# Kernel optimization log

Hardware: AMD Instinct MI355X
Metric: run time of the kernel (lower is better)

Reference implementation:

```python
import jax, jax.numpy as jnp
import numpy as np

EMBED_DIM = 768
NUM_HEADS = 12
HEAD_DIM = EMBED_DIM // NUM_HEADS


def setup_inputs() -> dict:
    key = jax.random.key(0)
    k1, k2, k3, k4, k5 = jax.random.split(key, 5)
    B, S, D = 2, 4096, EMBED_DIM
    scale = 1.0 / np.sqrt(D)
    return {
        "x": jax.random.normal(k1, (B, S, D), dtype=jnp.float32),
        "Wqkv": jax.random.normal(k2, (D, 3 * D), dtype=jnp.float32) * scale,
        "bqkv": jax.random.normal(k3, (3 * D,), dtype=jnp.float32) * 0.02,
        "Wout": jax.random.normal(k4, (D, D), dtype=jnp.float32) * scale,
        "bout": jax.random.normal(k5, (D,), dtype=jnp.float32) * 0.02,
    }


def reference(x, Wqkv, bqkv, Wout, bout):
    B, S, D = x.shape
    H, Hd = NUM_HEADS, HEAD_DIM
    # fused QKV projection: [B,S,3D]
    qkv = x @ Wqkv + bqkv
    q, k, v = jnp.split(qkv, 3, axis=-1)
    # [B,S,D] -> [B,H,S,Hd]
    q = q.reshape(B, S, H, Hd).transpose(0, 2, 1, 3)
    k = k.reshape(B, S, H, Hd).transpose(0, 2, 1, 3)
    v = v.reshape(B, S, H, Hd).transpose(0, 2, 1, 3)
    # causal SDPA (dropout_p = 0)
    scores = jnp.einsum("bhsd,bhtd->bhst", q, k) / jnp.sqrt(jnp.asarray(Hd, x.dtype))
    causal = jnp.tril(jnp.ones((S, S), dtype=bool))  # [S,S]
    scores = jnp.where(causal[None, None], scores, jnp.finfo(x.dtype).min)
    attn = jax.nn.softmax(scores, axis=-1)
    y = jnp.einsum("bhst,bhtd->bhsd", attn, v)  # [B,H,S,Hd]
    y = y.transpose(0, 2, 1, 3).reshape(B, S, D)
    return y @ Wout + bout
```

## Files before the change

kernel.cpp:

```cpp
#include <hip/hip_runtime.h>

#define S_LEN 4096
#define NH 12
#define HD 64
#define DMODEL 768
#define BATCH 2
#define MTOT (BATCH * S_LEN)

typedef __bf16 bf16x8 __attribute__((ext_vector_type(8)));
typedef __bf16 bf16x4 __attribute__((ext_vector_type(4)));
typedef float f32x4 __attribute__((ext_vector_type(4)));
typedef float f32x8 __attribute__((ext_vector_type(8)));

#define SM_SCALE_LOG2E 0.18033688f
#define SLAB_STRIDE 16896

__device__ __forceinline__ f32x4 f32x4_zero() {
  f32x4 z = {0.f, 0.f, 0.f, 0.f};
  return z;
}

__device__ __forceinline__ void async16(const __bf16* g, void* l) {
  __builtin_amdgcn_global_load_lds(
      (const __attribute__((address_space(1))) void*)g,
      (__attribute__((address_space(3))) void*)l, 16, 0, 0);
}

__global__ __launch_bounds__(256) void prep_all(const float* __restrict__ x,
                                                const float* __restrict__ Wqkv,
                                                const float* __restrict__ Wout,
                                                __bf16* __restrict__ xb,
                                                __bf16* __restrict__ Wqkv_t,
                                                __bf16* __restrict__ Wout_t) {
  __shared__ __bf16 t[64][72];
  const int bid = blockIdx.x;
  if (bid < 3072) {
    int i = bid * 256 + threadIdx.x;
    f32x8 a = ((const f32x8*)x)[i];
    bf16x8 o;
#pragma unroll
    for (int j = 0; j < 8; ++j) o[j] = (__bf16)a[j];
    ((bf16x8*)xb)[i] = o;
    return;
  }
  const float* in;
  __bf16* out;
  int N, v;
  if (bid < 3504) {
    in = Wqkv;
    out = Wqkv_t;
    N = 3 * DMODEL;
    v = bid - 3072;
  } else {
    in = Wout;
    out = Wout_t;
    N = DMODEL;
    v = bid - 3504;
  }
  int kb = (v % 12) * 64, nb = (v / 12) * 64;
  int c = threadIdx.x & 63, r0 = threadIdx.x >> 6;
#pragma unroll
  for (int i = 0; i < 16; ++i) {
    int r = r0 * 16 + i;
    t[c][r] = (__bf16)in[(size_t)(kb + r) * N + nb + c];
  }
  __syncthreads();
#pragma unroll
  for (int i = 0; i < 16; ++i) {
    int r = r0 * 16 + i;
    out[(size_t)(nb + r) * DMODEL + kb + c] = t[r][c];
  }
}

__device__ __forceinline__ void gemm128_bt(const __bf16* __restrict__ A,
                                           const __bf16* __restrict__ Bt,
                                           int m0, int n0, int K,
                                           __bf16* Alds, __bf16* Blds,
                                           f32x4 acc[4][4]) {
  const int tid = threadIdx.x;
  const int l = tid & 63, w = tid >> 6;
  const int wr = w >> 1, wc = w & 1;
  const int g = l >> 4, ln = l & 15;

  const int rr = tid >> 3;
  const int sx = (tid & 7) ^ (rr & 7);
  const __bf16* As = A + (size_t)(m0 + rr) * K + sx * 8;
  const __bf16* Bs = Bt + (size_t)(n0 + rr) * K + sx * 8;
  char* Ad = (char*)Alds + (w << 10);
  char* Bd = (char*)Blds + (w << 10);

  for (int k0 = 0; k0 < K; k0 += 64) {
#pragma unroll
    for (int i = 0; i < 4; ++i) {
      async16(As + (size_t)(i * 32) * K + k0, Ad + i * 4096);
      async16(Bs + (size_t)(i * 32) * K + k0, Bd + i * 4096);
    }
    __syncthreads();
#pragma unroll
    for (int kk = 0; kk < 2; ++kk) {
      bf16x8 af[4], bfr[4];
#pragma unroll
      for (int mi = 0; mi < 4; ++mi) {
        int row = wr * 64 + mi * 16 + ln;
        af[mi] = *(const bf16x8*)(Alds + row * 64 + ((((kk << 2) + g) ^ (row & 7)) << 3));
      }
#pragma unroll
      for (int ni = 0; ni < 4; ++ni) {
        int row = wc * 64 + ni * 16 + ln;
        bfr[ni] = *(const bf16x8*)(Blds + row * 64 + ((((kk << 2) + g) ^ (row & 7)) << 3));
      }
#pragma unroll
      for (int mi = 0; mi < 4; ++mi)
#pragma unroll
        for (int ni = 0; ni < 4; ++ni)
          acc[mi][ni] =
              __builtin_amdgcn_mfma_f32_16x16x32_bf16(af[mi], bfr[ni], acc[mi][ni], 0, 0, 0);
    }
    __syncthreads();
  }
}

__global__ __launch_bounds__(256) void gemm_qkv(const __bf16* __restrict__ xb,
                                                const __bf16* __restrict__ Wt,
                                                const float* __restrict__ bqkv,
                                                __bf16* __restrict__ Qo,
                                                __bf16* __restrict__ Ko,
                                                __bf16* __restrict__ Vto) {
  __shared__ __bf16 Alds[128 * 64];
  __shared__ __bf16 Blds[128 * 64];
  int bm = blockIdx.x & 63, bn = blockIdx.x >> 6;
  int m0 = bm * 128, n0 = bn * 128;
  f32x4 acc[4][4];
#pragma unroll
  for (int i = 0; i < 4; ++i)
#pragma unroll
    for (int j = 0; j < 4; ++j) acc[i][j] = f32x4_zero();
  gemm128_bt(xb, Wt, m0, n0, DMODEL, Alds, Blds, acc);

  const int l = threadIdx.x & 63, w = threadIdx.x >> 6;
  const int wr = w >> 1, wc = w & 1, g = l >> 4, ln = l & 15;
#pragma unroll
  for (int ni = 0; ni < 4; ++ni) {
    int ncol = n0 + wc * 64 + ni * 16 + ln;
    int which = ncol / DMODEL;
    int dd = ncol - which * DMODEL;
    int h = dd >> 6, hd = dd & 63;
    float bias = bqkv[ncol];
    if (which == 2) {
#pragma unroll
      for (int mi = 0; mi < 4; ++mi)
#pragma unroll
        for (int r = 0; r < 4; ++r) {
          int mrow = m0 + wr * 64 + mi * 16 + 4 * g + r;
          int b = mrow >> 12, s = mrow & (S_LEN - 1);
          float v = acc[mi][ni][r] + bias;
          Vto[(((size_t)(b * NH + h) * HD) + hd) * S_LEN + s] = (__bf16)v;
        }
    } else {
      __bf16* op = (which == 0) ? Qo : Ko;
      const float scl = (which == 0) ? SM_SCALE_LOG2E : 1.0f;
#pragma unroll
      for (int mi = 0; mi < 4; ++mi)
#pragma unroll
        for (int r = 0; r < 4; ++r) {
          int mrow = m0 + wr * 64 + mi * 16 + 4 * g + r;
          int b = mrow >> 12, s = mrow & (S_LEN - 1);
          float v = (acc[mi][ni][r] + bias) * scl;
          op[((((size_t)b * NH + h) * S_LEN) + s) * HD + hd] = (__bf16)v;
        }
    }
  }
}

__global__ __launch_bounds__(256) void gemm_out(const __bf16* __restrict__ yb,
                                                const __bf16* __restrict__ Wt,
                                                const float* __restrict__ bout,
                                                float* __restrict__ out) {
  __shared__ __bf16 Alds[128 * 64];
  __shared__ __bf16 Blds[128 * 64];
  int bm = blockIdx.x & 63, bn = blockIdx.x >> 6;
  int m0 = bm * 128, n0 = bn * 128;
  f32x4 acc[4][4];
#pragma unroll
  for (int i = 0; i < 4; ++i)
#pragma unroll
    for (int j = 0; j < 4; ++j) acc[i][j] = f32x4_zero();
  gemm128_bt(yb, Wt, m0, n0, DMODEL, Alds, Blds, acc);

  const int l = threadIdx.x & 63, w = threadIdx.x >> 6;
  const int wr = w >> 1, wc = w & 1, g = l >> 4, ln = l & 15;
#pragma unroll
  for (int ni = 0; ni < 4; ++ni) {
    int ncol = n0 + wc * 64 + ni * 16 + ln;
    float bias = bout[ncol];
#pragma unroll
    for (int mi = 0; mi < 4; ++mi)
#pragma unroll
      for (int r = 0; r < 4; ++r) {
        int mrow = m0 + wr * 64 + mi * 16 + 4 * g + r;
        out[(size_t)mrow * DMODEL + ncol] = acc[mi][ni][r] + bias;
      }
  }
}

__global__ __launch_bounds__(512) void attn_fwd18(const __bf16* __restrict__ Q,
                                                  const __bf16* __restrict__ K,
                                                  const __bf16* __restrict__ Vt,
                                                  __bf16* __restrict__ Y,
                                                  char* __restrict__ Po) {
  __shared__ __bf16 KVl[2][2][4096];
  __shared__ char Plb[8][2048];

  const int tid = threadIdx.x;
  const int wv = tid >> 6, l = tid & 63;
  const int g = l >> 4, ln = l & 15;
  const int bi = blockIdx.x;
  const int xcd = bi & 7, j = bi >> 3;
  const int head = xcd * 3 + (j % 3);
  const int r_ = j / 3;

  int c, part, np;
  bool split;
  if (r_ < 32) {
    c = 31 - (r_ >> 2);
    part = r_ & 3;
    np = 4;
    split = true;
  } else if (r_ < 56) {
    int q = r_ - 32;
    c = 23 - q / 3;
    part = q % 3;
    np = 3;
    split = true;
  } else if (r_ < 72) {
    int q = r_ - 56;
    c = 15 - (q >> 1);
    part = q & 1;
    np = 2;
    split = true;
  } else {
    c = 79 - r_;
    part = 0;
    np = 1;
    split = false;
  }
  const int T = 2 * c + 2;
  const int base = T / np, rem = T % np;
  const int t0 = part * base + (part < rem ? part : rem);
  const int t1 = t0 + base + (part < rem ? 1 : 0);

  const int q0 = 128 * c + 16 * wv;

  const size_t hb = (size_t)head * (S_LEN * HD);
  const __bf16* Qh = Q + hb;
  const __bf16* Kh = K + hb;
  const __bf16* Vh = Vt + hb;

  const int sw = (ln & 7) << 4;
  char* Pw = Plb[wv] + ln * 128;

  const int r0 = tid >> 3;
  const int s0 = (tid & 7) ^ (r0 & 7);
  const size_t kL = (size_t)r0 * HD + s0 * 8;
  const size_t vL = (size_t)r0 * S_LEN + s0 * 8;
  const int ldsoff = wv << 10;

  bf16x8 qf[2];
#pragma unroll
  for (int t = 0; t < 2; ++t)
    qf[t] = *(const bf16x8*)(Qh + (size_t)(q0 + ln) * HD + 32 * t + 8 * g);

  bf16x8 ones;
#pragma unroll
  for (int t = 0; t < 8; ++t) ones[t] = (__bf16)1.0f;

  f32x4 o[4], o5;
#pragma unroll
  for (int nt = 0; nt < 4; ++nt) o[nt] = f32x4_zero();
  o5 = f32x4_zero();

  const __bf16* kq = Kh + (size_t)t0 * 64 * HD;
  const __bf16* vq = Vh + t0 * 64;
  {
    async16(kq + kL, (char*)&KVl[0][0][0] + ldsoff);
    async16(vq + vL, (char*)&KVl[0][1][0] + ldsoff);
    __syncthreads();
  }
  kq += (size_t)64 * HD;
  vq += 64;

  int cur = 0;
  for (int i = t0; i < t1; ++i) {
    const bool more = (i + 1) < t1;
    if (more) {
      async16(kq + kL, (char*)&KVl[cur ^ 1][0][0] + ldsoff);
      async16(vq + vL, (char*)&KVl[cur ^ 1][1][0] + ldsoff);
      kq += (size_t)64 * HD;
      vq += 64;
    }

    const __bf16* Kl = &KVl[cur][0][0];
    const __bf16* Vl = &KVl[cur][1][0];
    const int rel = q0 - 64 * i;

    if (rel > -16) {
      if (rel >= 63) {
#pragma unroll
        for (int jt = 0; jt < 4; ++jt) {
          int row = 16 * jt + ln;
          bf16x8 kf0 = *(const bf16x8*)(Kl + row * 64 + ((g ^ (row & 7)) << 3));
          bf16x8 kf1 = *(const bf16x8*)(Kl + row * 64 + (((4 + g) ^ (row & 7)) << 3));
          f32x4 z = f32x4_zero();
          z = __builtin_amdgcn_mfma_f32_16x16x32_bf16(kf0, qf[0], z, 0, 0, 0);
          z = __builtin_amdgcn_mfma_f32_16x16x32_bf16(kf1, qf[1], z, 0, 0, 0);
          bf16x4 qd;
#pragma unroll
          for (int r = 0; r < 4; ++r) qd[r] = (__bf16)__builtin_exp2f(z[r]);
          *(bf16x4*)(Pw + ((32 * jt + 8 * g) ^ sw)) = qd;
        }
      } else {
        const int thr = rel + ln;
#pragma unroll
        for (int jt = 0; jt < 4; ++jt) {
          int row = 16 * jt + ln;
          bf16x8 kf0 = *(const bf16x8*)(Kl + row * 64 + ((g ^ (row & 7)) << 3));
          bf16x8 kf1 = *(const bf16x8*)(Kl + row * 64 + (((4 + g) ^ (row & 7)) << 3));
          f32x4 z = f32x4_zero();
          z = __builtin_amdgcn_mfma_f32_16x16x32_bf16(kf0, qf[0], z, 0, 0, 0);
          z = __builtin_amdgcn_mfma_f32_16x16x32_bf16(kf1, qf[1], z, 0, 0, 0);
          bf16x4 qd;
#pragma unroll
          for (int r = 0; r < 4; ++r) {
            float pv = __builtin_exp2f(z[r]);
            if (16 * jt + 4 * g + r > thr) pv = 0.f;
            qd[r] = (__bf16)pv;
          }
          *(bf16x4*)(Pw + ((32 * jt + 8 * g) ^ sw)) = qd;
        }
      }

      bf16x8 pa0 = *(const bf16x8*)(Pw + ((16 * g) ^ sw));
      bf16x8 pa1 = *(const bf16x8*)(Pw + ((64 + 16 * g) ^ sw));
      __builtin_amdgcn_s_setprio(1);
      o5 = __builtin_amdgcn_mfma_f32_16x16x32_bf16(pa0, ones, o5, 0, 0, 0);
      o5 = __builtin_amdgcn_mfma_f32_16x16x32_bf16(pa1, ones, o5, 0, 0, 0);
#pragma unroll
      for (int nt = 0; nt < 4; ++nt) {
        int row = 16 * nt + ln;
        bf16x8 vf0 = *(const bf16x8*)(Vl + row * 64 + ((g ^ (row & 7)) << 3));
        bf16x8 vf1 = *(const bf16x8*)(Vl + row * 64 + (((4 + g) ^ (row & 7)) << 3));
        o[nt] = __builtin_amdgcn_mfma_f32_16x16x32_bf16(pa0, vf0, o[nt], 0, 0, 0);
        o[nt] = __builtin_amdgcn_mfma_f32_16x16x32_bf16(pa1, vf1, o[nt], 0, 0, 0);
      }
      __builtin_amdgcn_s_setprio(0);
    }

    if (more) __syncthreads();
    cur ^= 1;
  }

  if (!split) {
    const int bb = head / NH, hh = head - bb * NH;
    __bf16* Yp = Y + ((size_t)bb * S_LEN) * DMODEL + hh * HD;
#pragma unroll
    for (int r = 0; r < 4; ++r) {
      float inv = 1.0f / o5[r];
      int qr = q0 + 4 * g + r;
#pragma unroll
      for (int nt = 0; nt < 4; ++nt)
        Yp[(size_t)qr * DMODEL + 16 * nt + ln] = (__bf16)(o[nt][r] * inv);
    }
  } else {
    int soff;
    if (c < 16) soff = (c - 8) * 2 + part;
    else if (c < 24) soff = 16 + (c - 16) * 3 + part;
    else soff = 40 + (c - 24) * 4 + part;
    char* slab = Po + ((size_t)head * 72 + soff) * SLAB_STRIDE;
#pragma unroll
    for (int r = 0; r < 4; ++r) {
      int rowL = 16 * wv + 4 * g + r;
#pragma unroll
      for (int nt = 0; nt < 4; ++nt)
        *(__bf16*)(slab + (rowL * 64 + 16 * nt + ln) * 2) = (__bf16)o[nt][r];
      if (ln == 0) *(float*)(slab + 16384 + rowL * 4) = o5[r];
    }
  }
}

__global__ __launch_bounds__(256) void attn_combine(const char* __restrict__ Po,
                                                    __bf16* __restrict__ Y) {
  const int blk = blockIdx.x;
  const int head = blk / 96, rem = blk - head * 96;
  const int cc = rem >> 2, quarter = rem & 3;
  const int c = cc + 8;
  int np, boff;
  if (c < 16) {
    np = 2;
    boff = (c - 8) * 2;
  } else if (c < 24) {
    np = 3;
    boff = 16 + (c - 16) * 3;
  } else {
    np = 4;
    boff = 40 + (c - 24) * 4;
  }
  const char* s = Po + ((size_t)head * 72 + boff) * SLAB_STRIDE;
  const int tid = threadIdx.x;
  const int row = quarter * 32 + (tid >> 3), d0 = (tid & 7) * 8;

  float acc[8] = {0.f, 0.f, 0.f, 0.f, 0.f, 0.f, 0.f, 0.f};
  float rs = 0.f;
  for (int p = 0; p < np; ++p) {
    bf16x8 a = *(const bf16x8*)(s + (size_t)p * SLAB_STRIDE + (row * 64 + d0) * 2);
#pragma unroll
    for (int j = 0; j < 8; ++j) acc[j] += (float)a[j];
    rs += *(const float*)(s + (size_t)p * SLAB_STRIDE + 16384 + row * 4);
  }
  float inv = 1.0f / rs;

  const int bb = head / NH, hh = head - bb * NH;
  __bf16* yp = Y + ((size_t)bb * S_LEN + 128 * c + row) * DMODEL + hh * HD + d0;
  bf16x8 o;
#pragma unroll
  for (int j = 0; j < 8; ++j) o[j] = (__bf16)(acc[j] * inv);
  *(bf16x8*)yp = o;
}

extern "C" void kernel_launch(void* const* d_in, const int* in_sizes, int n_in,
                              void* d_out, int out_size, void* d_ws, size_t ws_size,
                              hipStream_t stream) {
  const float* x = (const float*)d_in[0];
  const float* Wqkv = (const float*)d_in[1];
  const float* bqkv = (const float*)d_in[2];
  const float* Wout = (const float*)d_in[3];
  const float* bout = (const float*)d_in[4];
  float* out = (float*)d_out;

  char* ws = (char*)d_ws;
  size_t off = 0;
  auto take = [&](size_t bytes) {
    char* p = ws + off;
    off += bytes;
    return p;
  };
  const size_t MD2 = (size_t)MTOT * DMODEL * 2;
  __bf16* xb = (__bf16*)take(MD2);
  __bf16* Wqkv_t = (__bf16*)take((size_t)3 * DMODEL * DMODEL * 2);
  __bf16* Wout_t = (__bf16*)take((size_t)DMODEL * DMODEL * 2);
  __bf16* Qb = (__bf16*)take(MD2);
  __bf16* Kb = (__bf16*)take(MD2);
  __bf16* Vtb = (__bf16*)take(MD2);
  __bf16* Yb = (__bf16*)take(MD2);
  char* Po = take((size_t)24 * 72 * SLAB_STRIDE);

  prep_all<<<3648, 256, 0, stream>>>(x, Wqkv, Wout, xb, Wqkv_t, Wout_t);
  gemm_qkv<<<64 * (3 * DMODEL / 128), 256, 0, stream>>>(xb, Wqkv_t, bqkv, Qb, Kb, Vtb);
  attn_fwd18<<<1920, 512, 0, stream>>>(Qb, Kb, Vtb, Yb, Po);
  attn_combine<<<2304, 256, 0, stream>>>(Po, Yb);
  gemm_out<<<64 * (DMODEL / 128), 256, 0, stream>>>(Yb, Wout_t, bout, out);
}
```

Before: 168.5 us.

## Single-buffer K tile with mid-iteration barrier, keep V double-buffered

K is now held in one LDS buffer instead of two. The next K tile is issued after a barrier placed between the QK^T/softmax phase and the PV phase, while V stays double-buffered. This cuts the attention kernel's LDS footprint, which may allow more blocks per CU and overlaps the K load with the PV MFMAs. The cost is an extra __syncthreads per iteration and less prefetch distance for K. Correctness relies on the loop-end barrier so the K load completes before the next iteration reads it.

After: 173.6 us. 1.03x slower.

```diff
diff --git a/kernel.cpp b/kernel.cpp
--- a/kernel.cpp
+++ b/kernel.cpp
@@ -203,12 +203,13 @@
   }
 }
 
-__global__ __launch_bounds__(512) void attn_fwd18(const __bf16* __restrict__ Q,
+__global__ __launch_bounds__(512) void attn_fwd21(const __bf16* __restrict__ Q,
                                                   const __bf16* __restrict__ K,
                                                   const __bf16* __restrict__ Vt,
                                                   __bf16* __restrict__ Y,
                                                   char* __restrict__ Po) {
-  __shared__ __bf16 KVl[2][2][4096];
+  __shared__ __bf16 Klds[4096];
+  __shared__ __bf16 Vlds[2][4096];
   __shared__ char Plb[8][2048];
 
   const int tid = threadIdx.x;
@@ -282,8 +283,8 @@
   const __bf16* kq = Kh + (size_t)t0 * 64 * HD;
   const __bf16* vq = Vh + t0 * 64;
   {
-    async16(kq + kL, (char*)&KVl[0][0][0] + ldsoff);
-    async16(vq + vL, (char*)&KVl[0][1][0] + ldsoff);
+    async16(kq + kL, (char*)Klds + ldsoff);
+    async16(vq + vL, (char*)&Vlds[0][0] + ldsoff);
     __syncthreads();
   }
   kq += (size_t)64 * HD;
@@ -293,14 +294,11 @@
   for (int i = t0; i < t1; ++i) {
     const bool more = (i + 1) < t1;
     if (more) {
-      async16(kq + kL, (char*)&KVl[cur ^ 1][0][0] + ldsoff);
-      async16(vq + vL, (char*)&KVl[cur ^ 1][1][0] + ldsoff);
-      kq += (size_t)64 * HD;
+      async16(vq + vL, (char*)&Vlds[cur ^ 1][0] + ldsoff);
       vq += 64;
     }
 
-    const __bf16* Kl = &KVl[cur][0][0];
-    const __bf16* Vl = &KVl[cur][1][0];
+    const __bf16* Vl = &Vlds[cur][0];
     const int rel = q0 - 64 * i;
 
     if (rel > -16) {
@@ -308,8 +306,8 @@
 #pragma unroll
         for (int jt = 0; jt < 4; ++jt) {
           int row = 16 * jt + ln;
-          bf16x8 kf0 = *(const bf16x8*)(Kl + row * 64 + ((g ^ (row & 7)) << 3));
-          bf16x8 kf1 = *(const bf16x8*)(Kl + row * 64 + (((4 + g) ^ (row & 7)) << 3));
+          bf16x8 kf0 = *(const bf16x8*)(Klds + row * 64 + ((g ^ (row & 7)) << 3));
+          bf16x8 kf1 = *(const bf16x8*)(Klds + row * 64 + (((4 + g) ^ (row & 7)) << 3));
           f32x4 z = f32x4_zero();
           z = __builtin_amdgcn_mfma_f32_16x16x32_bf16(kf0, qf[0], z, 0, 0, 0);
           z = __builtin_amdgcn_mfma_f32_16x16x32_bf16(kf1, qf[1], z, 0, 0, 0);
@@ -323,8 +321,8 @@
 #pragma unroll
         for (int jt = 0; jt < 4; ++jt) {
           int row = 16 * jt + ln;
-          bf16x8 kf0 = *(const bf16x8*)(Kl + row * 64 + ((g ^ (row & 7)) << 3));
-          bf16x8 kf1 = *(const bf16x8*)(Kl + row * 64 + (((4 + g) ^ (row & 7)) << 3));
+          bf16x8 kf0 = *(const bf16x8*)(Klds + row * 64 + ((g ^ (row & 7)) << 3));
+          bf16x8 kf1 = *(const bf16x8*)(Klds + row * 64 + (((4 + g) ^ (row & 7)) << 3));
           f32x4 z = f32x4_zero();
           z = __builtin_amdgcn_mfma_f32_16x16x32_bf16(kf0, qf[0], z, 0, 0, 0);
           z = __builtin_amdgcn_mfma_f32_16x16x32_bf16(kf1, qf[1], z, 0, 0, 0);
@@ -338,7 +336,15 @@
           *(bf16x4*)(Pw + ((32 * jt + 8 * g) ^ sw)) = qd;
         }
       }
-
+    }
+
+    if (more) {
+      __syncthreads();
+      async16(kq + kL, (char*)Klds + ldsoff);
+      kq += (size_t)64 * HD;
+    }
+
+    if (rel > -16) {
       bf16x8 pa0 = *(const bf16x8*)(Pw + ((16 * g) ^ sw));
       bf16x8 pa1 = *(const bf16x8*)(Pw + ((64 + 16 * g) ^ sw));
       __builtin_amdgcn_s_setprio(1);
@@ -455,7 +461,7 @@
 
   prep_all<<<3648, 256, 0, stream>>>(x, Wqkv, Wout, xb, Wqkv_t, Wout_t);
   gemm_qkv<<<64 * (3 * DMODEL / 128), 256, 0, stream>>>(xb, Wqkv_t, bqkv, Qb, Kb, Vtb);
-  attn_fwd18<<<1920, 512, 0, stream>>>(Qb, Kb, Vtb, Yb, Po);
+  attn_fwd21<<<1920, 512, 0, stream>>>(Qb, Kb, Vtb, Yb, Po);
   attn_combine<<<2304, 256, 0, stream>>>(Po, Yb);
   gemm_out<<<64 * (DMODEL / 128), 256, 0, stream>>>(Yb, Wout_t, bout, out);
 }
```
